# Performance work log

Measured on AMD Instinct MI355X. Metric: run time of the kernel, lower is better.

Reference implementation:

```python
import jax, jax.numpy as jnp
import numpy as np
import itertools

K = 10            # knn size in GFM
SHARP = 20.0      # GMCCE_Sharp
THRES = 0.5       # GMCCE_Thres
EPS = 1e-6
P_EPS = 1e-7      # procrustes epsilon
_COMB = np.array(list(itertools.combinations(range(K), 2)))  # (45,2)


def _tri_areas_sorted(pcd, tri):
    # pcd: (B,N,3) points; tri: (B,N,P,3) int vertex indices -> (B,N,P,3)
    g = jax.vmap(lambda p, t: p[t])(pcd, tri)        # (B,N,P,3,3)
    e1 = g[..., 1, :] - g[..., 0, :]
    e2 = g[..., 2, :] - g[..., 0, :]
    areas = 0.5 * jnp.linalg.norm(jnp.cross(e1, e2), axis=-1)  # (B,N,P)
    z = jnp.zeros_like(areas)
    # original stores area in channel 0 of a zero (.,.,.,3) buffer then sorts ascending
    return jnp.sort(jnp.stack([areas, z, z], axis=-1), axis=-1)


def _gfm(src, tgt):
    # src: (B,3,N); tgt: (B,N,3) -> 0/1 weights (B,N)
    B, _, N = src.shape
    p = jnp.swapaxes(src, 1, 2)                       # (B,N,3)
    sq = jnp.sum(p * p, axis=-1)
    d2 = sq[:, :, None] + sq[:, None, :] - 2.0 * jnp.einsum('bnd,bmd->bnm', p, p)
    w = jnp.exp(-jnp.maximum(d2, 0.0) / 2.0)          # sigma=1; cdist**2 == d2
    _, knn_idx = jax.lax.top_k(w, K)                  # (B,N,K) nearest (incl. self)
    pairs = knn_idx[:, :, _COMB]                      # (B,N,45,2)
    n_p = _COMB.shape[0]
    self_idx = jnp.broadcast_to(jnp.arange(N)[None, :, None, None], (B, N, n_p, 1))
    tri = jnp.concatenate([self_idx, pairs], axis=-1) # (B,N,45,3)
    sl = _tri_areas_sorted(p, tri)
    tl = _tri_areas_sorted(tgt, tri) + EPS
    loss = jnp.sum((sl - tl) ** 2, axis=-1) / jnp.sum(sl + tl, axis=-1)  # (B,N,45)
    sorted_loss = jnp.sort(loss, axis=-1)
    reg = jnp.linalg.norm(sl - tl, axis=-1)
    total = sorted_loss + 0.1 * reg
    med = jnp.median(total, axis=-1, keepdims=True)
    total = jnp.where(total > 3.0 * med, 0.0, total)
    limited = jnp.sqrt(total[:, :, :K] + EPS)
    mean_loss = jnp.mean(limited, axis=-1)            # (B,N)
    min_loss = jnp.min(mean_loss, axis=-1, keepdims=True)
    wts = 2.0 * jax.nn.sigmoid(-SHARP * (mean_loss - min_loss))
    return jnp.where(wts > THRES, 1.0, 0.0)


def _procrustes(X, Y, w):
    # X,Y: (N,3); w: (N,1) weights (detached in original)
    tw = jnp.sum(jnp.abs(w))
    nw = jnp.broadcast_to(w.reshape(-1, 1), X.shape) / (tw + P_EPS)
    mx = jnp.sum(nw * X, axis=0, keepdims=True)       # (1,3)
    my = jnp.sum(nw * Y, axis=0, keepdims=True)
    cov = (Y - my).T @ (nw * (X - mx))                # (3,3)
    U, _, Vh = jnp.linalg.svd(cov)
    sign = jnp.where(jnp.linalg.det(U) * jnp.linalg.det(Vh) < 0, -1.0, 1.0)
    S = jnp.diag(jnp.stack([jnp.ones(()), jnp.ones(()), sign]))
    R = U @ S @ Vh
    # faithful to original: (3,) - (3,1) broadcasts to (3,3)
    T = my.reshape(3) - R @ mx.T
    return R, T


def setup_inputs() -> dict:
    key = jax.random.key(0)
    k1, k2, k3, k4, k5 = jax.random.split(key, 5)
    B, D, N = 8, 512, 2048
    return {
        'src_embedding': jax.random.normal(k1, (B, D, N), dtype=jnp.float32),
        'tgt_embedding': jax.random.normal(k2, (B, D, N), dtype=jnp.float32),
        'src': jax.random.normal(k3, (B, 3, N), dtype=jnp.float32),
        'tgt': jax.random.normal(k4, (B, 3, N), dtype=jnp.float32),
        'temperature': jax.random.uniform(k5, (B, 1), dtype=jnp.float32),
        'is_corr': 1,
    }


def reference(src_embedding, tgt_embedding, src, tgt, temperature, is_corr):
    d_k = src_embedding.shape[1]
    scores = jnp.einsum('bdn,bdm->bnm', src_embedding, tgt_embedding) / jnp.sqrt(jnp.float32(d_k))
    scores = jax.nn.softmax(10000.0 * scores, axis=2)  # (B,N,N)
    corres = jnp.argmax(scores, axis=-1)               # (B,N)
    tgt_t = jnp.swapaxes(tgt, 1, 2)                    # (B,N,3)
    src_t = jnp.swapaxes(src, 1, 2)
    corr_tgt = jnp.einsum('bnm,bmd->bnd', scores, tgt_t)
    weight = _gfm(src, corr_tgt)[..., None]            # (B,N,1)
    src_corr = jnp.take_along_axis(tgt_t, corres[..., None], axis=1)  # (B,N,3)
    R, T = jax.vmap(_procrustes)(src_t, src_corr, jax.lax.stop_gradient(weight))
    return R, T, corres[..., None], weight
```

## Files before the change

### kernel.cpp

```cpp
#include <hip/hip_runtime.h>
#include <math.h>

#define BATCH 8
#define DIM   512
#define NPTS  2048
#define KNN   10
#define NPAIR 45
#define FCHK   32
#define FCHKSZ 64

typedef __attribute__((ext_vector_type(8))) short    bf16x8;
typedef __attribute__((ext_vector_type(4))) float    f32x4;
typedef __attribute__((ext_vector_type(4))) unsigned int u32x4;

__device__ inline unsigned short bf16_rne(float x) {
    unsigned int u = __float_as_uint(x);
    u += 0x7FFFu + ((u >> 16) & 1u);
    return (unsigned short)(u >> 16);
}
__device__ inline float bf16_to_f(unsigned short h) {
    return __uint_as_float(((unsigned int)h) << 16);
}
__device__ inline unsigned long long shflx_u64(unsigned long long v, int mask) {
    unsigned int lo = (unsigned int)v, hi = (unsigned int)(v >> 32);
    lo = (unsigned int)__shfl_xor((int)lo, mask);
    hi = (unsigned int)__shfl_xor((int)hi, mask);
    return ((unsigned long long)hi << 32) | lo;
}

__global__ __launch_bounds__(256)
void split_kernel(const float* __restrict__ se, const float* __restrict__ te,
                  unsigned short* __restrict__ pA, unsigned short* __restrict__ pB)
{
    const int bid = blockIdx.x;
    const int tensor = bid >> 11;
    const int rr_ = bid & 2047;
    const int b  = rr_ >> 8;
    const int dt = (rr_ >> 5) & 7;
    const int nt = rr_ & 31;
    const float* srcp = (tensor == 0 ? se : te)
                        + ((size_t)b * DIM + dt * 64) * NPTS + nt * 64;
    unsigned short* dst = (tensor == 0 ? pA : pB);
    const size_t PL = (size_t)BATCH * NPTS * DIM;
    unsigned short* base = dst + (size_t)b * NPTS * DIM + (size_t)nt * 64 * DIM + dt * 64;

    __shared__ float T[64][65];
    const int t = threadIdx.x;
    {
        int r = t >> 4, c4 = t & 15;
        #pragma unroll
        for (int it = 0; it < 4; ++it) {
            int d = r + it * 16;
            float4 v = *(const float4*)&srcp[(size_t)d * NPTS + c4 * 4];
            T[d][c4 * 4 + 0] = v.x; T[d][c4 * 4 + 1] = v.y;
            T[d][c4 * 4 + 2] = v.z; T[d][c4 * 4 + 3] = v.w;
        }
    }
    __syncthreads();
    const int n  = t >> 2;
    const int d0 = (t & 3) * 16;
    unsigned short hh[16], mm[16], ll[16];
    #pragma unroll
    for (int j = 0; j < 16; ++j) {
        float a = T[d0 + j][n];
        unsigned short h = bf16_rne(a);
        float r1 = a - bf16_to_f(h);
        unsigned short m = bf16_rne(r1);
        float r2 = r1 - bf16_to_f(m);
        unsigned short l = bf16_rne(r2);
        hh[j] = h; mm[j] = m; ll[j] = l;
    }
    unsigned short* o = base + (size_t)n * DIM + d0;
    *(u32x4*)(o)            = *(u32x4*)&hh[0];
    *(u32x4*)(o + 8)        = *(u32x4*)&hh[8];
    *(u32x4*)(o + PL)       = *(u32x4*)&mm[0];
    *(u32x4*)(o + PL + 8)   = *(u32x4*)&mm[8];
    *(u32x4*)(o + 2*PL)     = *(u32x4*)&ll[0];
    *(u32x4*)(o + 2*PL + 8) = *(u32x4*)&ll[8];
}

__global__ __launch_bounds__(256, 2)
void score_h(const unsigned short* __restrict__ pA, const unsigned short* __restrict__ pB,
             unsigned short* __restrict__ uhat)
{
    const int bid  = blockIdx.x;
    const int xcd  = bid & 7;
    const int slot = bid >> 3;
    const int g    = xcd + 8 * (slot >> 4);
    const int ntile = slot & 15;
    const int b    = g >> 2;
    const int mc   = g & 3;
    const int n0 = ntile * 128;
    const int t  = threadIdx.x;
    const int w  = t >> 6;
    const int l  = t & 63;
    const int wn = w >> 1, wm = w & 1;
    const int l15 = l & 15, l4 = l >> 4;

    __shared__ unsigned short As[128 * 64];
    __shared__ unsigned short Bs[128 * 64];

    int srow[4], skg[4], ldsoff[4];
    #pragma unroll
    for (int qq = 0; qq < 4; ++qq) {
        int s = qq * 256 + t;
        int row = s >> 3, slt = s & 7;
        srow[qq] = row;
        skg[qq] = slt ^ (row & 7);
        ldsoff[qq] = row * 64 + slt * 8;
    }
    int aroff[4], arxor[4], broff[4], brxor[4];
    #pragma unroll
    for (int i = 0; i < 4; ++i) {
        int ar = wn * 64 + i * 16 + l15;
        aroff[i] = ar * 64; arxor[i] = ar & 7;
        int br = wm * 64 + i * 16 + l15;
        broff[i] = br * 64; brxor[i] = br & 7;
    }

    const float scl = 10000.0f / sqrtf((float)DIM);
    const unsigned short* Ab = pA + (size_t)b * NPTS * DIM;
    const unsigned short* Bb = pB + (size_t)b * NPTS * DIM;

    for (int mt = 0; mt < 4; ++mt) {
        const int m0 = mc * 512 + mt * 128;
        f32x4 acc[4][4];
        #pragma unroll
        for (int i = 0; i < 4; ++i)
            #pragma unroll
            for (int j = 0; j < 4; ++j) acc[i][j] = (f32x4){0.f, 0.f, 0.f, 0.f};

        for (int k0 = 0; k0 < 512; k0 += 64) {
            __syncthreads();
            bf16x8 ra[4], rb[4];
            #pragma unroll
            for (int qq = 0; qq < 4; ++qq) {
                ra[qq] = *(const bf16x8*)&Ab[(size_t)(n0 + srow[qq]) * DIM + k0 + skg[qq] * 8];
                rb[qq] = *(const bf16x8*)&Bb[(size_t)(m0 + srow[qq]) * DIM + k0 + skg[qq] * 8];
            }
            #pragma unroll
            for (int qq = 0; qq < 4; ++qq) {
                *(bf16x8*)&As[ldsoff[qq]] = ra[qq];
                *(bf16x8*)&Bs[ldsoff[qq]] = rb[qq];
            }
            __syncthreads();
            #pragma unroll
            for (int ks = 0; ks < 2; ++ks) {
                bf16x8 af[4], bfr[4];
                #pragma unroll
                for (int i = 0; i < 4; ++i) {
                    af[i]  = *(const bf16x8*)&As[aroff[i] + (((ks * 4 + l4) ^ arxor[i]) * 8)];
                    bfr[i] = *(const bf16x8*)&Bs[broff[i] + (((ks * 4 + l4) ^ brxor[i]) * 8)];
                }
                #pragma unroll
                for (int i = 0; i < 4; ++i)
                    #pragma unroll
                    for (int j = 0; j < 4; ++j)
                        acc[i][j] = __builtin_amdgcn_mfma_f32_16x16x32_bf16(af[i], bfr[j], acc[i][j], 0, 0, 0);
            }
        }
        #pragma unroll
        for (int i = 0; i < 4; ++i) {
            #pragma unroll
            for (int j = 0; j < 4; ++j) {
                int mcol = m0 + wm * 64 + j * 16 + l15;
                #pragma unroll
                for (int r = 0; r < 4; ++r) {
                    int nabs = n0 + wn * 64 + i * 16 + l4 * 4 + r;
                    uhat[((size_t)(b * NPTS + nabs)) * NPTS + mcol] =
                        bf16_rne(scl * acc[i][j][r]);
                }
            }
        }
    }
}

__global__ __launch_bounds__(256)
void resolve(const unsigned short* __restrict__ uhat,
             const unsigned short* __restrict__ pA, const unsigned short* __restrict__ pB,
             const float* __restrict__ tgt,
             float* __restrict__ corr_tgt, int* __restrict__ corres_i,
             float* __restrict__ corres_out)
{
    const int wid  = threadIdx.x >> 6;
    const int lane = threadIdx.x & 63;
    const int gid  = blockIdx.x * 4 + wid;
    const int b    = gid >> 11;
    const int n    = gid & 2047;

    __shared__ int s_m[4][64];
    __shared__ int s_cnt[4];

    if (lane == 0) s_cnt[wid] = 0;
    __syncthreads();

    const unsigned short* urow = uhat + (size_t)gid * NPTS;
    float v[32];
    float lmax = -3.402823466e38f; int lk = 0;
    #pragma unroll
    for (int g2 = 0; g2 < 4; ++g2) {
        u32x4 pk = *(const u32x4*)&urow[lane * 32 + g2 * 8];
        #pragma unroll
        for (int e = 0; e < 4; ++e) {
            unsigned int w2 = pk[e];
            float f0 = __uint_as_float((w2 & 0xFFFFu) << 16);
            float f1 = __uint_as_float(w2 & 0xFFFF0000u);
            int k0 = g2 * 8 + e * 2;
            v[k0] = f0; v[k0 + 1] = f1;
            if (f0 > lmax) { lmax = f0; lk = k0; }
            if (f1 > lmax) { lmax = f1; lk = k0 + 1; }
        }
    }
    float vmax = lmax; int argm = lane * 32 + lk;
    #pragma unroll
    for (int mask = 1; mask < 64; mask <<= 1) {
        float ov = __shfl_xor(vmax, mask);
        int   oi = __shfl_xor(argm, mask);
        if (ov > vmax || (ov == vmax && oi < argm)) { vmax = ov; argm = oi; }
    }
    const float cut = vmax - 1200.0f;
    int cnt = 0;
    #pragma unroll
    for (int k = 0; k < 32; ++k) cnt += (v[k] >= cut) ? 1 : 0;
    int nc = cnt;
    #pragma unroll
    for (int mask = 1; mask < 64; mask <<= 1) nc += __shfl_xor(nc, mask);

    if (nc > 1) {
        #pragma unroll
        for (int k = 0; k < 32; ++k) {
            if (v[k] >= cut) {
                int slot = atomicAdd(&s_cnt[wid], 1);
                if (slot < 64) s_m[wid][slot] = lane * 32 + k;
            }
        }
    }
    __syncthreads();
    if (nc > 1 && lane == 0) {
        int ncc = nc > 64 ? 64 : nc;
        for (int i = 1; i < ncc; ++i) {
            int key = s_m[wid][i]; int j = i - 1;
            while (j >= 0 && s_m[wid][j] > key) { s_m[wid][j + 1] = s_m[wid][j]; --j; }
            s_m[wid][j + 1] = key;
        }
    }
    __syncthreads();

    if (nc == 1) {
        if (lane < 3) corr_tgt[(size_t)gid * 3 + lane] = tgt[((size_t)b * 3 + lane) * NPTS + argm];
        if (lane == 0) { corres_i[gid] = argm; corres_out[gid] = (float)argm; }
        return;
    }
    const int ncc = nc > 64 ? 64 : nc;

    const size_t PL = (size_t)BATCH * NPTS * DIM;
    const unsigned short* Ar = pA + ((size_t)b * NPTS + n) * DIM + lane * 8;
    bf16x8 a_h = *(const bf16x8*)&Ar[0];
    bf16x8 a_m = *(const bf16x8*)&Ar[PL];
    bf16x8 a_l = *(const bf16x8*)&Ar[2 * PL];
    float ah[8], am[8], al[8];
    #pragma unroll
    for (int e = 0; e < 8; ++e) {
        ah[e] = bf16_to_f((unsigned short)a_h[e]);
        am[e] = bf16_to_f((unsigned short)a_m[e]);
        al[e] = bf16_to_f((unsigned short)a_l[e]);
    }

    const float sqd = sqrtf((float)DIM);
    float umax = -3.402823466e38f; int uarg = 0x7fffffff;
    float myu = 0.f;
    for (int c = 0; c < ncc; ++c) {
        int mB = s_m[wid][c];
        const unsigned short* Br = pB + ((size_t)b * NPTS + mB) * DIM + lane * 8;
        bf16x8 b_h = *(const bf16x8*)&Br[0];
        bf16x8 b_m = *(const bf16x8*)&Br[PL];
        bf16x8 b_l = *(const bf16x8*)&Br[2 * PL];
        float part = 0.f;
        #pragma unroll
        for (int e = 0; e < 8; ++e) {
            float bh = bf16_to_f((unsigned short)b_h[e]);
            float bm = bf16_to_f((unsigned short)b_m[e]);
            float bl = bf16_to_f((unsigned short)b_l[e]);
            part += ah[e] * bh;
            part += ah[e] * bm;
            part += am[e] * bh;
            part += ah[e] * bl;
            part += am[e] * bm;
            part += al[e] * bh;
        }
        #pragma unroll
        for (int mask = 1; mask < 64; mask <<= 1) part += __shfl_xor(part, mask);
        float u = 10000.0f * (part / sqd);
        if (u > umax) { umax = u; uarg = mB; }
        if (lane == c) myu = u;
    }

    float p = (lane < ncc) ? expf(myu - umax) : 0.f;
    int myM = (lane < ncc) ? s_m[wid][lane] : 0;
    float tx = 0.f, ty = 0.f, tz = 0.f, ps = p;
    if (lane < ncc) {
        tx = p * tgt[((size_t)b * 3 + 0) * NPTS + myM];
        ty = p * tgt[((size_t)b * 3 + 1) * NPTS + myM];
        tz = p * tgt[((size_t)b * 3 + 2) * NPTS + myM];
    }
    #pragma unroll
    for (int mask = 1; mask < 64; mask <<= 1) {
        ps += __shfl_xor(ps, mask);
        tx += __shfl_xor(tx, mask);
        ty += __shfl_xor(ty, mask);
        tz += __shfl_xor(tz, mask);
    }
    if (lane == 0) {
        corr_tgt[(size_t)gid * 3 + 0] = tx / ps;
        corr_tgt[(size_t)gid * 3 + 1] = ty / ps;
        corr_tgt[(size_t)gid * 3 + 2] = tz / ps;
        corres_i[gid]   = uarg;
        corres_out[gid] = (float)uarg;
    }
}

__global__ __launch_bounds__(256, 2)
void score_mfma(const unsigned short* __restrict__ pA, const unsigned short* __restrict__ pB,
                const float* __restrict__ tgt, float* __restrict__ part)
{
    const int bid  = blockIdx.x;
    const int xcd  = bid & 7;
    const int slot = bid >> 3;
    const int g    = xcd + 8 * (slot >> 4);
    const int ntile = slot & 15;
    const int b    = g >> 2;
    const int mc   = g & 3;
    const int n0 = ntile * 128;
    const int t  = threadIdx.x;
    const int w  = t >> 6;
    const int l  = t & 63;
    const int wn = w >> 1, wm = w & 1;
    const int l15 = l & 15, l4 = l >> 4;

    __shared__ unsigned short As[128 * 64];
    __shared__ unsigned short Bs[128 * 64];

    const size_t PL = (size_t)BATCH * NPTS * DIM;

    int srow[4], skg[4], ldsoff[4];
    #pragma unroll
    for (int qq = 0; qq < 4; ++qq) {
        int s = qq * 256 + t;
        int row = s >> 3, slt = s & 7;
        srow[qq] = row;
        skg[qq] = slt ^ (row & 7);
        ldsoff[qq] = row * 64 + slt * 8;
    }
    int aroff[4], arxor[4], broff[4], brxor[4];
    #pragma unroll
    for (int i = 0; i < 4; ++i) {
        int ar = wn * 64 + i * 16 + l15;
        aroff[i] = ar * 64; arxor[i] = ar & 7;
        int br = wm * 64 + i * 16 + l15;
        broff[i] = br * 64; brxor[i] = br & 7;
    }

    float mx[16], sm[16], ax[16], ay[16], az[16]; int ag[16];
    #pragma unroll
    for (int si = 0; si < 16; ++si) {
        mx[si] = -3.402823466e38f; sm[si] = 0.f;
        ax[si] = 0.f; ay[si] = 0.f; az[si] = 0.f; ag[si] = 0;
    }

    const float sqd = sqrtf((float)DIM);
    const unsigned short* Ab = pA + (size_t)b * NPTS * DIM;
    const unsigned short* Bb = pB + (size_t)b * NPTS * DIM;
    const int AIDX[6] = {0, 0, 1, 0, 1, 2};
    const int BIDX[6] = {0, 1, 0, 2, 1, 0};

    for (int mt = 0; mt < 4; ++mt) {
        const int m0 = mc * 512 + mt * 128;
        f32x4 acc[4][4];
        #pragma unroll
        for (int i = 0; i < 4; ++i)
            #pragma unroll
            for (int j = 0; j < 4; ++j) acc[i][j] = (f32x4){0.f, 0.f, 0.f, 0.f};

        for (int q = 0; q < 6; ++q) {
            const unsigned short* Ap = Ab + (size_t)AIDX[q] * PL;
            const unsigned short* Bp = Bb + (size_t)BIDX[q] * PL;
            for (int k0 = 0; k0 < 512; k0 += 64) {
                __syncthreads();
                bf16x8 ra[4], rb[4];
                #pragma unroll
                for (int qq = 0; qq < 4; ++qq) {
                    ra[qq] = *(const bf16x8*)&Ap[(size_t)(n0 + srow[qq]) * DIM + k0 + skg[qq] * 8];
                    rb[qq] = *(const bf16x8*)&Bp[(size_t)(m0 + srow[qq]) * DIM + k0 + skg[qq] * 8];
                }
                #pragma unroll
                for (int qq = 0; qq < 4; ++qq) {
                    *(bf16x8*)&As[ldsoff[qq]] = ra[qq];
                    *(bf16x8*)&Bs[ldsoff[qq]] = rb[qq];
                }
                __syncthreads();
                #pragma unroll
                for (int ks = 0; ks < 2; ++ks) {
                    bf16x8 af[4], bfr[4];
                    #pragma unroll
                    for (int i = 0; i < 4; ++i) {
                        af[i]  = *(const bf16x8*)&As[aroff[i] + (((ks * 4 + l4) ^ arxor[i]) * 8)];
                        bfr[i] = *(const bf16x8*)&Bs[broff[i] + (((ks * 4 + l4) ^ brxor[i]) * 8)];
                    }
                    #pragma unroll
                    for (int i = 0; i < 4; ++i)
                        #pragma unroll
                        for (int j = 0; j < 4; ++j)
                            acc[i][j] = __builtin_amdgcn_mfma_f32_16x16x32_bf16(af[i], bfr[j], acc[i][j], 0, 0, 0);
                }
            }
        }
        float tg0[4], tg1[4], tg2[4];
        #pragma unroll
        for (int j = 0; j < 4; ++j) {
            int mcol = m0 + wm * 64 + j * 16 + l15;
            tg0[j] = tgt[((size_t)b * 3 + 0) * NPTS + mcol];
            tg1[j] = tgt[((size_t)b * 3 + 1) * NPTS + mcol];
            tg2[j] = tgt[((size_t)b * 3 + 2) * NPTS + mcol];
        }
        #pragma unroll
        for (int i = 0; i < 4; ++i) {
            #pragma unroll
            for (int r = 0; r < 4; ++r) {
                const int si = i * 4 + r;
                float u[4];
                float lm = -3.402823466e38f; int la = 0;
                #pragma unroll
                for (int j = 0; j < 4; ++j) {
                    float s  = acc[i][j][r] / sqd;
                    float uu = 10000.0f * s;
                    u[j] = uu;
                    if (uu > lm) { lm = uu; la = m0 + wm * 64 + j * 16 + l15; }
                }
                float nm = fmaxf(mx[si], lm);
                if (lm > mx[si]) ag[si] = la;
                float f = expf(mx[si] - nm);
                mx[si] = nm;
                float s_ = sm[si] * f, x_ = ax[si] * f, y_ = ay[si] * f, z_ = az[si] * f;
                #pragma unroll
                for (int j = 0; j < 4; ++j) {
                    float p = expf(u[j] - nm);
                    s_ += p; x_ += p * tg0[j]; y_ += p * tg1[j]; z_ += p * tg2[j];
                }
                sm[si] = s_; ax[si] = x_; ay[si] = y_; az[si] = z_;
            }
        }
    }

    #pragma unroll
    for (int si = 0; si < 16; ++si) {
        for (int mask = 1; mask < 16; mask <<= 1) {
            float omx = __shfl_xor(mx[si], mask);
            float osm = __shfl_xor(sm[si], mask);
            float oax = __shfl_xor(ax[si], mask);
            float oay = __shfl_xor(ay[si], mask);
            float oaz = __shfl_xor(az[si], mask);
            int   oag = __shfl_xor(ag[si], mask);
            float nm = fmaxf(mx[si], omx);
            float f1 = expf(mx[si] - nm), f2 = expf(omx - nm);
            sm[si] = sm[si] * f1 + osm * f2;
            ax[si] = ax[si] * f1 + oax * f2;
            ay[si] = ay[si] * f1 + oay * f2;
            az[si] = az[si] * f1 + oaz * f2;
            ag[si] = (omx > mx[si]) ? oag : ((omx == mx[si]) ? min(ag[si], oag) : ag[si]);
            mx[si] = nm;
        }
    }
    if (l15 == 0) {
        const int chunk = mc * 2 + wm;
        #pragma unroll
        for (int i = 0; i < 4; ++i)
            #pragma unroll
            for (int r = 0; r < 4; ++r) {
                const int si = i * 4 + r;
                int nabs = n0 + wn * 64 + i * 16 + l4 * 4 + r;
                size_t o = (((size_t)b * NPTS + nabs) * 8 + chunk) * 8;
                part[o + 0] = mx[si]; part[o + 1] = sm[si];
                part[o + 2] = ax[si]; part[o + 3] = ay[si]; part[o + 4] = az[si];
                part[o + 5] = __int_as_float(ag[si]);
            }
    }
}

__global__ __launch_bounds__(256)
void merge8_kernel(const float* __restrict__ part, float* __restrict__ corr_tgt,
                   int* __restrict__ corres_i, float* __restrict__ corres_out)
{
    int r = blockIdx.x * 256 + threadIdx.x;
    float m = -3.402823466e38f, s = 0.f, x = 0.f, y = 0.f, z = 0.f; int a = 0x7fffffff;
    for (int c = 0; c < 8; ++c) {
        const float* p = &part[((size_t)r * 8 + c) * 8];
        float pm = p[0]; int pa = __float_as_int(p[5]);
        float nm = fmaxf(m, pm);
        float f1 = expf(m - nm), f2 = expf(pm - nm);
        s = s * f1 + p[1] * f2;
        x = x * f1 + p[2] * f2;
        y = y * f1 + p[3] * f2;
        z = z * f1 + p[4] * f2;
        if (pm > m) a = pa; else if (pm == m) a = min(a, pa);
        m = nm;
    }
    corr_tgt[(size_t)r * 3 + 0] = x / s;
    corr_tgt[(size_t)r * 3 + 1] = y / s;
    corr_tgt[(size_t)r * 3 + 2] = z / s;
    corres_i[r]   = a;
    corres_out[r] = (float)a;
}

__global__ __launch_bounds__(256)
void prep_p4(const float* __restrict__ src, float4* __restrict__ P4)
{
    int i = blockIdx.x * 256 + threadIdx.x;
    int b = i >> 11, m = i & 2047;
    float x = src[((size_t)b * 3 + 0) * NPTS + m];
    float y = src[((size_t)b * 3 + 1) * NPTS + m];
    float z = src[((size_t)b * 3 + 2) * NPTS + m];
    P4[i] = make_float4(x, y, z, x * x + y * y + z * z);
}

__global__ __launch_bounds__(256)
void knn_topk(const float4* __restrict__ P4, int* __restrict__ topI)
{
    const int bid = blockIdx.x;
    const int b = bid >> 8, nblk = bid & 255;
    const int t = threadIdx.x;
    const int c  = t & (FCHK - 1);
    const int rl = t >> 5;
    const int n = nblk * 8 + rl;
    const float4* Pb = P4 + (size_t)b * NPTS;
    const float4 pn = Pb[n];

    unsigned int kx[KNN], ix[KNN];
    #pragma unroll
    for (int k = 0; k < KNN; ++k) { kx[k] = 0xFFFFFFFFu; ix[k] = 0xFFFFFFFFu; }

    const int m0 = c * FCHKSZ;
    for (int mm = 0; mm < FCHKSZ; ++mm) {
        int m = m0 + mm;
        float4 pm = Pb[m];
        float dot = pn.x * pm.x + pn.y * pm.y + pn.z * pm.z;
        float d2  = (pn.w + pm.w) - 2.0f * dot;
        if (d2 < 0.f) d2 = 0.f;
        float w = expf(-d2 * 0.5f);
        unsigned int key = ~__float_as_uint(w);
        if (key < kx[KNN - 1]) {
            unsigned int ck = key, ci = (unsigned int)m;
            #pragma unroll
            for (int k = 0; k < KNN; ++k) {
                bool lt = ck < kx[k];
                unsigned int tk = kx[k], ti = ix[k];
                kx[k] = lt ? ck : kx[k];
                ix[k] = lt ? ci : ix[k];
                ck = lt ? tk : ck;
                ci = lt ? ti : ci;
            }
        }
    }

    unsigned long long kl[KNN];
    #pragma unroll
    for (int k = 0; k < KNN; ++k)
        kl[k] = ((unsigned long long)kx[k] << 32) | ix[k];

    #pragma unroll
    for (int mask = 1; mask < FCHK; mask <<= 1) {
        unsigned long long B[KNN];
        #pragma unroll
        for (int k = 0; k < KNN; ++k) B[k] = shflx_u64(kl[k], mask);
        unsigned long long M[KNN];
        #pragma unroll
        for (int k = 0; k < KNN; ++k) {
            unsigned long long best = B[k];
            #pragma unroll
            for (int i = 1; i <= k; ++i) {
                unsigned long long hi = kl[i - 1] > B[k - i] ? kl[i - 1] : B[k - i];
                best = hi < best ? hi : best;
            }
            unsigned long long ak = kl[k];
            M[k] = ak < best ? ak : best;
        }
        #pragma unroll
        for (int k = 0; k < KNN; ++k) kl[k] = M[k];
    }

    if (c == 0) {
        size_t gid = (size_t)(b << 11) + n;
        #pragma unroll
        for (int k = 0; k < KNN; ++k)
            topI[gid * KNN + k] = (int)(kl[k] & 0xFFFFFFFFull);
    }
}

__global__ __launch_bounds__(256)
void gfm_finish(const float4* __restrict__ P4, const float* __restrict__ corr_tgt,
                const int* __restrict__ topI, float* __restrict__ mean_loss)
{
    const int wid  = threadIdx.x >> 6;
    const int lane = threadIdx.x & 63;
    const int gid  = blockIdx.x * 4 + wid;
    const int b    = gid >> 11;

    __shared__ float PT[4][KNN][6];
    __shared__ float LS[4][48];
    __shared__ float SR[4][48];
    __shared__ float TOT[4][48];

    if (lane < KNN) {
        int idx = topI[(size_t)gid * KNN + lane];
        float4 pk = P4[(b << 11) + idx];
        size_t o = ((size_t)(b << 11) + idx) * 3;
        PT[wid][lane][0] = pk.x; PT[wid][lane][1] = pk.y; PT[wid][lane][2] = pk.z;
        PT[wid][lane][3] = corr_tgt[o];
        PT[wid][lane][4] = corr_tgt[o + 1];
        PT[wid][lane][5] = corr_tgt[o + 2];
    }
    float4 pn = P4[gid];
    size_t on = (size_t)gid * 3;
    const float cnx = corr_tgt[on], cny = corr_tgt[on + 1], cnz = corr_tgt[on + 2];
    __syncthreads();

    int pi = 0, pj = 1;
    {
        int pp = lane;
        #pragma unroll
        for (int r = 0; r < 9; ++r) {
            int cnt = 9 - r;
            if (pp >= 0 && pp < cnt) { pi = r; pj = r + 1 + pp; }
            pp -= cnt;
        }
    }

    float ls_p = 0.f, rg_p = 0.f;
    if (lane < NPAIR) {
        float e1x = PT[wid][pi][0] - pn.x, e1y = PT[wid][pi][1] - pn.y, e1z = PT[wid][pi][2] - pn.z;
        float e2x = PT[wid][pj][0] - pn.x, e2y = PT[wid][pj][1] - pn.y, e2z = PT[wid][pj][2] - pn.z;
        float cx = e1y * e2z - e1z * e2y;
        float cy = e1z * e2x - e1x * e2z;
        float cz = e1x * e2y - e1y * e2x;
        float as_ = 0.5f * sqrtf(cx * cx + cy * cy + cz * cz);
        float f1x = PT[wid][pi][3] - cnx, f1y = PT[wid][pi][4] - cny, f1z = PT[wid][pi][5] - cnz;
        float f2x = PT[wid][pj][3] - cnx, f2y = PT[wid][pj][4] - cny, f2z = PT[wid][pj][5] - cnz;
        float gx = f1y * f2z - f1z * f2y;
        float gy = f1z * f2x - f1x * f2z;
        float gz = f1x * f2y - f1y * f2x;
        float at_ = 0.5f * sqrtf(gx * gx + gy * gy + gz * gz);
        float tl2 = at_ + 1e-6f;
        float dd  = as_ - tl2;
        float e2_ = 1e-6f * 1e-6f;
        float num = (e2_ + e2_) + dd * dd;
        float den = (1e-6f + 1e-6f) + (as_ + tl2);
        ls_p = num / den;
        rg_p = sqrtf(num);
        LS[wid][lane] = ls_p;
    }
    __syncthreads();

    int rk = 0;
    if (lane < NPAIR) {
        #pragma unroll
        for (int q = 0; q < NPAIR; ++q) {
            float lq = LS[wid][q];
            rk += (lq < ls_p) || (lq == ls_p && q < lane);
        }
        SR[wid][rk] = ls_p;
    }
    __syncthreads();

    float tot_p = 0.f;
    if (lane < NPAIR) {
        tot_p = SR[wid][lane] + 0.1f * rg_p;
        TOT[wid][lane] = tot_p;
    }
    __syncthreads();

    int rt2 = 0;
    if (lane < NPAIR) {
        #pragma unroll
        for (int q = 0; q < NPAIR; ++q) {
            float tq = TOT[wid][q];
            rt2 += (tq < tot_p) || (tq == tot_p && q < lane);
        }
        SR[wid][rt2] = tot_p;
    }
    __syncthreads();

    float med = SR[wid][22];
    float thr = 3.0f * med;
    if (lane < KNN) {
        float v = tot_p;
        v = (v > thr) ? 0.0f : v;
        LS[wid][lane] = sqrtf(v + 1e-6f);
    }
    __syncthreads();
    if (lane == 0) {
        float acc = 0.f;
        #pragma unroll
        for (int k = 0; k < KNN; ++k) acc += LS[wid][k];
        mean_loss[gid] = acc / 10.0f;
    }
}

__global__ __launch_bounds__(256)
void weight_kernel(const float* __restrict__ mean_loss, float* __restrict__ weight_out)
{
    const int b = blockIdx.x;
    const int t = threadIdx.x;
    __shared__ float red[256];
    float mn = 3.402823466e38f;
    for (int i = t; i < NPTS; i += 256)
        mn = fminf(mn, mean_loss[(size_t)b * NPTS + i]);
    red[t] = mn; __syncthreads();
    for (int s2 = 128; s2 > 0; s2 >>= 1) {
        if (t < s2) red[t] = fminf(red[t], red[t + s2]);
        __syncthreads();
    }
    float ml = red[0];
    for (int i = t; i < NPTS; i += 256) {
        float d = mean_loss[(size_t)b * NPTS + i] - ml;
        float e = expf(-20.0f * d);
        float wts = 2.0f * (e / (1.0f + e));
        weight_out[(size_t)b * NPTS + i] = (wts > 0.5f) ? 1.0f : 0.0f;
    }
}

__device__ void jacobi4(double A[4][4], double V[4][4]) {
    for (int i = 0; i < 4; ++i)
        for (int j = 0; j < 4; ++j) V[i][j] = (i == j) ? 1.0 : 0.0;
    for (int sweep = 0; sweep < 12; ++sweep) {
        for (int p = 0; p < 3; ++p) for (int q = p + 1; q < 4; ++q) {
            double apq = A[p][q];
            if (fabs(apq) < 1e-30) continue;
            double theta = (A[q][q] - A[p][p]) / (2.0 * apq);
            double tt = (theta >= 0 ? 1.0 : -1.0) / (fabs(theta) + sqrt(theta * theta + 1.0));
            double c = 1.0 / sqrt(tt * tt + 1.0), s = tt * c;
            for (int k = 0; k < 4; ++k) {
                double akp = A[k][p], akq = A[k][q];
                A[k][p] = c * akp - s * akq;
                A[k][q] = s * akp + c * akq;
            }
            for (int k = 0; k < 4; ++k) {
                double apk = A[p][k], aqk = A[q][k];
                A[p][k] = c * apk - s * aqk;
                A[q][k] = s * apk + c * aqk;
            }
            for (int k = 0; k < 4; ++k) {
                double vkp = V[k][p], vkq = V[k][q];
                V[k][p] = c * vkp - s * vkq;
                V[k][q] = s * vkp + c * vkq;
            }
        }
    }
}

__global__ __launch_bounds__(256)
void procrustes_kernel(const float* __restrict__ src, const float* __restrict__ tgt,
                       const int* __restrict__ corres_i, const float* __restrict__ weight,
                       float* __restrict__ outR, float* __restrict__ outT)
{
    const int b = blockIdx.x;
    const int t = threadIdx.x;
    __shared__ float red[256][9];
    __shared__ float s_tw, s_mx[3], s_my[3];
    __shared__ float s_cov[9];

    float a0 = 0, a1 = 0, a2 = 0, a3 = 0, a4 = 0, a5 = 0, a6 = 0;
    for (int i = t; i < NPTS; i += 256) {
        float w = weight[(size_t)b * NPTS + i];
        float X0 = src[((size_t)b * 3 + 0) * NPTS + i];
        float X1 = src[((size_t)b * 3 + 1) * NPTS + i];
        float X2 = src[((size_t)b * 3 + 2) * NPTS + i];
        int c = corres_i[(size_t)b * NPTS + i];
        float Y0 = tgt[((size_t)b * 3 + 0) * NPTS + c];
        float Y1 = tgt[((size_t)b * 3 + 1) * NPTS + c];
        float Y2 = tgt[((size_t)b * 3 + 2) * NPTS + c];
        a0 += w;
        a1 += w * X0; a2 += w * X1; a3 += w * X2;
        a4 += w * Y0; a5 += w * Y1; a6 += w * Y2;
    }
    red[t][0] = a0; red[t][1] = a1; red[t][2] = a2; red[t][3] = a3;
    red[t][4] = a4; red[t][5] = a5; red[t][6] = a6; red[t][7] = 0; red[t][8] = 0;
    __syncthreads();
    for (int s2 = 128; s2 > 0; s2 >>= 1) {
        if (t < s2)
            for (int k = 0; k < 7; ++k) red[t][k] += red[t + s2][k];
        __syncthreads();
    }
    if (t == 0) {
        float tw = red[0][0];
        float itw = tw + 1e-7f;
        s_tw = tw;
        s_mx[0] = red[0][1] / itw; s_mx[1] = red[0][2] / itw; s_mx[2] = red[0][3] / itw;
        s_my[0] = red[0][4] / itw; s_my[1] = red[0][5] / itw; s_my[2] = red[0][6] / itw;
    }
    __syncthreads();
    const float twp = s_tw + 1e-7f;
    const float mx0 = s_mx[0], mx1 = s_mx[1], mx2 = s_mx[2];
    const float my0 = s_my[0], my1 = s_my[1], my2 = s_my[2];

    float cv[9] = {0,0,0,0,0,0,0,0,0};
    for (int i = t; i < NPTS; i += 256) {
        float w = weight[(size_t)b * NPTS + i];
        float nwn = w / twp;
        float X0 = src[((size_t)b * 3 + 0) * NPTS + i] - mx0;
        float X1 = src[((size_t)b * 3 + 1) * NPTS + i] - mx1;
        float X2 = src[((size_t)b * 3 + 2) * NPTS + i] - mx2;
        int c = corres_i[(size_t)b * NPTS + i];
        float Y0 = tgt[((size_t)b * 3 + 0) * NPTS + c] - my0;
        float Y1 = tgt[((size_t)b * 3 + 1) * NPTS + c] - my1;
        float Y2 = tgt[((size_t)b * 3 + 2) * NPTS + c] - my2;
        float b0 = nwn * X0, b1 = nwn * X1, b2 = nwn * X2;
        cv[0] += Y0 * b0; cv[1] += Y0 * b1; cv[2] += Y0 * b2;
        cv[3] += Y1 * b0; cv[4] += Y1 * b1; cv[5] += Y1 * b2;
        cv[6] += Y2 * b0; cv[7] += Y2 * b1; cv[8] += Y2 * b2;
    }
    __syncthreads();
    for (int k = 0; k < 9; ++k) red[t][k] = cv[k];
    __syncthreads();
    for (int s2 = 128; s2 > 0; s2 >>= 1) {
        if (t < s2)
            for (int k = 0; k < 9; ++k) red[t][k] += red[t + s2][k];
        __syncthreads();
    }
    if (t == 0) for (int k = 0; k < 9; ++k) s_cov[k] = red[0][k];
    __syncthreads();

    if (t == 0) {
        double cov[3][3];
        for (int i = 0; i < 3; ++i)
            for (int j = 0; j < 3; ++j) cov[i][j] = (double)s_cov[i * 3 + j];
        double S[3][3];
        for (int a = 0; a < 3; ++a)
            for (int bb = 0; bb < 3; ++bb) S[a][bb] = cov[bb][a];
        double N4[4][4];
        N4[0][0] = S[0][0] + S[1][1] + S[2][2];
        N4[0][1] = S[1][2] - S[2][1];
        N4[0][2] = S[2][0] - S[0][2];
        N4[0][3] = S[0][1] - S[1][0];
        N4[1][1] = S[0][0] - S[1][1] - S[2][2];
        N4[1][2] = S[0][1] + S[1][0];
        N4[1][3] = S[2][0] + S[0][2];
        N4[2][2] = -S[0][0] + S[1][1] - S[2][2];
        N4[2][3] = S[1][2] + S[2][1];
        N4[3][3] = -S[0][0] - S[1][1] + S[2][2];
        N4[1][0] = N4[0][1]; N4[2][0] = N4[0][2]; N4[3][0] = N4[0][3];
        N4[2][1] = N4[1][2]; N4[3][1] = N4[1][3]; N4[3][2] = N4[2][3];
        double V[4][4];
        jacobi4(N4, V);
        int best = 0; double bl = N4[0][0];
        for (int k = 1; k < 4; ++k) if (N4[k][k] > bl) { bl = N4[k][k]; best = k; }
        double q0 = V[0][best], qx = V[1][best], qy = V[2][best], qz = V[3][best];
        double nq = sqrt(q0 * q0 + qx * qx + qy * qy + qz * qz);
        q0 /= nq; qx /= nq; qy /= nq; qz /= nq;
        double Rm[3][3];
        Rm[0][0] = q0*q0 + qx*qx - qy*qy - qz*qz;
        Rm[0][1] = 2.0 * (qx*qy - q0*qz);
        Rm[0][2] = 2.0 * (qx*qz + q0*qy);
        Rm[1][0] = 2.0 * (qx*qy + q0*qz);
        Rm[1][1] = q0*q0 - qx*qx + qy*qy - qz*qz;
        Rm[1][2] = 2.0 * (qy*qz - q0*qx);
        Rm[2][0] = 2.0 * (qx*qz - q0*qy);
        Rm[2][1] = 2.0 * (qy*qz + q0*qx);
        Rm[2][2] = q0*q0 - qx*qx - qy*qy + qz*qz;
        double o1 = 0, o2 = 0;
        for (int i = 0; i < 3; ++i)
            for (int j = 0; j < 3; ++j) { o1 += Rm[i][j] * cov[i][j]; o2 += Rm[j][i] * cov[i][j]; }
        if (o2 > o1) {
            for (int i = 0; i < 3; ++i)
                for (int j = i + 1; j < 3; ++j) {
                    double tv = Rm[i][j]; Rm[i][j] = Rm[j][i]; Rm[j][i] = tv;
                }
        }
        float Rf[3][3];
        for (int i = 0; i < 3; ++i)
            for (int j = 0; j < 3; ++j) {
                Rf[i][j] = (float)Rm[i][j];
                outR[(size_t)b * 9 + i * 3 + j] = Rf[i][j];
            }
        float rm[3];
        float mxv[3] = {mx0, mx1, mx2};
        float myv[3] = {my0, my1, my2};
        for (int i = 0; i < 3; ++i)
            rm[i] = Rf[i][0] * mxv[0] + Rf[i][1] * mxv[1] + Rf[i][2] * mxv[2];
        for (int i = 0; i < 3; ++i)
            for (int j = 0; j < 3; ++j)
                outT[(size_t)b * 9 + i * 3 + j] = myv[j] - rm[i];
    }
}

extern "C" void kernel_launch(void* const* d_in, const int* in_sizes, int n_in,
                              void* d_out, int out_size, void* d_ws, size_t ws_size,
                              hipStream_t stream)
{
    const float* se  = (const float*)d_in[0];
    const float* te  = (const float*)d_in[1];
    const float* src = (const float*)d_in[2];
    const float* tgt = (const float*)d_in[3];

    float* out  = (float*)d_out;
    float* outR = out;
    float* outT = out + 72;
    float* outC = out + 144;
    float* outW = out + 144 + BATCH * NPTS;

    char* wsb = (char*)d_ws;
    float* corr_tgt  = (float*)wsb;
    int*   corres_i  = (int*)(wsb + 196608);
    float* mean_loss = (float*)(wsb + 262144);
    float* part      = (float*)(wsb + 327680);

    float4* P4   = (float4*)(wsb + 327680);
    int*    topI = (int*)(wsb + 589824);

    const size_t PLANES_OFF = 4521984;
    const size_t PL_BYTES   = (size_t)3 * BATCH * NPTS * DIM * 2;
    const size_t NEED       = PLANES_OFF + 2 * PL_BYTES;
    const size_t UHAT_BYTES = (size_t)BATCH * NPTS * NPTS * 2;
    const size_t NEED2      = NEED + UHAT_BYTES;

    unsigned short* pA = (unsigned short*)(wsb + PLANES_OFF);
    unsigned short* pB = (unsigned short*)(wsb + PLANES_OFF + PL_BYTES);
    unsigned short* uhat = (unsigned short*)(wsb + NEED);

    hipLaunchKernelGGL(split_kernel, dim3(4096), dim3(256), 0, stream, se, te, pA, pB);
    if (ws_size >= NEED2) {
        hipLaunchKernelGGL(score_h, dim3(512), dim3(256), 0, stream, pA, pB, uhat);
        hipLaunchKernelGGL(resolve, dim3(BATCH * NPTS / 4), dim3(256), 0, stream,
                           uhat, pA, pB, tgt, corr_tgt, corres_i, outC);
    } else {
        hipLaunchKernelGGL(score_mfma, dim3(512), dim3(256), 0, stream, pA, pB, tgt, part);
        hipLaunchKernelGGL(merge8_kernel, dim3(BATCH * NPTS / 256), dim3(256), 0, stream,
                           part, corr_tgt, corres_i, outC);
    }
    hipLaunchKernelGGL(prep_p4, dim3(BATCH * NPTS / 256), dim3(256), 0, stream, src, P4);
    hipLaunchKernelGGL(knn_topk, dim3(BATCH * 256), dim3(256), 0, stream, P4, topI);
    hipLaunchKernelGGL(gfm_finish, dim3(BATCH * NPTS / 4), dim3(256), 0, stream,
                       P4, corr_tgt, topI, mean_loss);
    hipLaunchKernelGGL(weight_kernel, dim3(BATCH), dim3(256), 0, stream,
                       mean_loss, outW);
    hipLaunchKernelGGL(procrustes_kernel, dim3(BATCH), dim3(256), 0, stream,
                       src, tgt, corres_i, outW, outR, outT);
}
```

Measured before the change: 262.7 us.

## Replace per-lane KNN insertion sort with threshold filter and shared candidate list

The kNN top-k kernel now finds a distance threshold in a first pass: each lane takes the minimum of its strided slice, then ten rounds of wave min-reduction give the 10th smallest lane-minimum, which bounds the true 10th nearest distance. A second pass recomputes distances, exps only points under that threshold, and appends them to a shared per-row buffer with atomics. Each lane then seeds a two-element list for the existing shuffle merge network, falling back to the old insertion sort if the buffer overflows. This removes the per-candidate sorted insertion and most expf calls, at the cost of a second pass over the points and LDS atomics.

```diff
diff --git a/kernel.cpp b/kernel.cpp
--- a/kernel.cpp
+++ b/kernel.cpp
@@ -6,8 +6,7 @@
 #define NPTS  2048
 #define KNN   10
 #define NPAIR 45
-#define FCHK   32
-#define FCHKSZ 64
+#define KCAP  64
 
 typedef __attribute__((ext_vector_type(8))) short    bf16x8;
 typedef __attribute__((ext_vector_type(4))) float    f32x4;
@@ -219,10 +218,10 @@
         if (ov > vmax || (ov == vmax && oi < argm)) { vmax = ov; argm = oi; }
     }
     const float cut = vmax - 1200.0f;
-    int cnt = 0;
-    #pragma unroll
-    for (int k = 0; k < 32; ++k) cnt += (v[k] >= cut) ? 1 : 0;
-    int nc = cnt;
+    int cnt2 = 0;
+    #pragma unroll
+    for (int k = 0; k < 32; ++k) cnt2 += (v[k] >= cut) ? 1 : 0;
+    int nc = cnt2;
     #pragma unroll
     for (int mask = 1; mask < 64; mask <<= 1) nc += __shfl_xor(nc, mask);
 
@@ -528,46 +527,95 @@
     const int bid = blockIdx.x;
     const int b = bid >> 8, nblk = bid & 255;
     const int t = threadIdx.x;
-    const int c  = t & (FCHK - 1);
+    const int c  = t & 31;
     const int rl = t >> 5;
     const int n = nblk * 8 + rl;
     const float4* Pb = P4 + (size_t)b * NPTS;
     const float4 pn = Pb[n];
 
-    unsigned int kx[KNN], ix[KNN];
-    #pragma unroll
-    for (int k = 0; k < KNN; ++k) { kx[k] = 0xFFFFFFFFu; ix[k] = 0xFFFFFFFFu; }
-
-    const int m0 = c * FCHKSZ;
-    for (int mm = 0; mm < FCHKSZ; ++mm) {
-        int m = m0 + mm;
+    __shared__ unsigned long long Lbuf[8][KCAP];
+    __shared__ int cnt[8];
+    if (c == 0) cnt[rl] = 0;
+    __syncthreads();
+
+    float lmin = 3.402823466e38f;
+    for (int i = 0; i < 64; ++i) {
+        int m = i * 32 + c;
         float4 pm = Pb[m];
         float dot = pn.x * pm.x + pn.y * pm.y + pn.z * pm.z;
-        float d2  = (pn.w + pm.w) - 2.0f * dot;
-        if (d2 < 0.f) d2 = 0.f;
-        float w = expf(-d2 * 0.5f);
-        unsigned int key = ~__float_as_uint(w);
-        if (key < kx[KNN - 1]) {
-            unsigned int ck = key, ci = (unsigned int)m;
-            #pragma unroll
-            for (int k = 0; k < KNN; ++k) {
-                bool lt = ck < kx[k];
-                unsigned int tk = kx[k], ti = ix[k];
-                kx[k] = lt ? ck : kx[k];
-                ix[k] = lt ? ci : ix[k];
-                ck = lt ? tk : ck;
-                ci = lt ? ti : ci;
-            }
-        }
-    }
+        float d2 = (pn.w + pm.w) - 2.0f * dot;
+        d2 = fmaxf(d2, 0.f);
+        lmin = fminf(lmin, d2);
+    }
+    float vv = lmin, Tt = 0.f;
+    for (int r = 0; r < 10; ++r) {
+        float gm = vv;
+        #pragma unroll
+        for (int mask = 1; mask < 32; mask <<= 1)
+            gm = fminf(gm, __shfl_xor(gm, mask));
+        Tt = gm;
+        vv = (vv == gm) ? 3.402823466e38f : vv;
+    }
+    const float Tp = Tt + 1e-4f;
+
+    for (int i = 0; i < 64; ++i) {
+        int m = i * 32 + c;
+        float4 pm = Pb[m];
+        float dot = pn.x * pm.x + pn.y * pm.y + pn.z * pm.z;
+        float d2 = (pn.w + pm.w) - 2.0f * dot;
+        d2 = fmaxf(d2, 0.f);
+        if (d2 <= Tp) {
+            float w = expf(-d2 * 0.5f);
+            unsigned long long key =
+                ((unsigned long long)(~__float_as_uint(w)) << 32) | (unsigned int)m;
+            int slot = atomicAdd(&cnt[rl], 1);
+            if (slot < KCAP) Lbuf[rl][slot] = key;
+        }
+    }
+    __syncthreads();
 
     unsigned long long kl[KNN];
-    #pragma unroll
-    for (int k = 0; k < KNN; ++k)
-        kl[k] = ((unsigned long long)kx[k] << 32) | ix[k];
-
-    #pragma unroll
-    for (int mask = 1; mask < FCHK; mask <<= 1) {
+    const int cr = cnt[rl];
+    if (cr <= KCAP) {
+        const unsigned long long UMAX = 0xFFFFFFFFFFFFFFFFull;
+        unsigned long long e0 = (c      < cr) ? Lbuf[rl][c]      : UMAX;
+        unsigned long long e1 = (c + 32 < cr) ? Lbuf[rl][c + 32] : UMAX;
+        kl[0] = e0 < e1 ? e0 : e1;
+        kl[1] = e0 < e1 ? e1 : e0;
+        #pragma unroll
+        for (int k = 2; k < KNN; ++k) kl[k] = UMAX;
+    } else {
+        unsigned int kx[KNN], ix[KNN];
+        #pragma unroll
+        for (int k = 0; k < KNN; ++k) { kx[k] = 0xFFFFFFFFu; ix[k] = 0xFFFFFFFFu; }
+        for (int i = 0; i < 64; ++i) {
+            int m = i * 32 + c;
+            float4 pm = Pb[m];
+            float dot = pn.x * pm.x + pn.y * pm.y + pn.z * pm.z;
+            float d2 = (pn.w + pm.w) - 2.0f * dot;
+            d2 = fmaxf(d2, 0.f);
+            float w = expf(-d2 * 0.5f);
+            unsigned int key = ~__float_as_uint(w);
+            if (key < kx[KNN - 1]) {
+                unsigned int ck = key, ci = (unsigned int)m;
+                #pragma unroll
+                for (int k = 0; k < KNN; ++k) {
+                    bool lt = ck < kx[k];
+                    unsigned int tk = kx[k], ti = ix[k];
+                    kx[k] = lt ? ck : kx[k];
+                    ix[k] = lt ? ci : ix[k];
+                    ck = lt ? tk : ck;
+                    ci = lt ? ti : ci;
+                }
+            }
+        }
+        #pragma unroll
+        for (int k = 0; k < KNN; ++k)
+            kl[k] = ((unsigned long long)kx[k] << 32) | ix[k];
+    }
+
+    #pragma unroll
+    for (int mask = 1; mask < 32; mask <<= 1) {
         unsigned long long B[KNN];
         #pragma unroll
         for (int k = 0; k < KNN; ++k) B[k] = shflx_u64(kl[k], mask);
@@ -628,9 +676,9 @@
         int pp = lane;
         #pragma unroll
         for (int r = 0; r < 9; ++r) {
-            int cnt = 9 - r;
-            if (pp >= 0 && pp < cnt) { pi = r; pj = r + 1 + pp; }
-            pp -= cnt;
+            int cnt3 = 9 - r;
+            if (pp >= 0 && pp < cnt3) { pi = r; pj = r + 1 + pp; }
+            pp -= cnt3;
         }
     }
 
```

Result: faster. 231.2 us (median of 2 runs) (-12.0%).
